# Optimization experiments

Measured on AMD Instinct MI355X. Metric: run time of the kernel, lower is better.

Reference implementation:

```python
import jax, jax.numpy as jnp
import numpy as np

EPS = 1e-08
CLAMP = 10.0


def setup_inputs() -> dict:
    key = jax.random.key(0)
    ks = jax.random.split(key, 16)
    B, T, F, H = 128, 512, 256, 512
    s_in = 1.0 / np.sqrt(F)
    s_h = 1.0 / np.sqrt(H)
    inp = {
        "x": jax.random.normal(ks[0], (B, T, F), dtype=jnp.float32),
        "Wf": jax.random.normal(ks[1], (F, H), dtype=jnp.float32) * s_in,
        "bf": jax.random.normal(ks[2], (H,), dtype=jnp.float32) * s_in,
        "Wi": jax.random.normal(ks[3], (F, H), dtype=jnp.float32) * s_in,
        "bi": jax.random.normal(ks[4], (H,), dtype=jnp.float32) * s_in,
        "Wo": jax.random.normal(ks[5], (F, H), dtype=jnp.float32) * s_in,
        "bo": jax.random.normal(ks[6], (H,), dtype=jnp.float32) * s_in,
        "Wz": jax.random.normal(ks[7], (F, H), dtype=jnp.float32) * s_in,
        "bz": jax.random.normal(ks[8], (H,), dtype=jnp.float32) * s_in,
        "Rf": jax.random.normal(ks[9], (H, H), dtype=jnp.float32) * s_h,
        "Ri": jax.random.normal(ks[10], (H, H), dtype=jnp.float32) * s_h,
        "Ro": jax.random.normal(ks[11], (H, H), dtype=jnp.float32) * s_h,
        "Rz": jax.random.normal(ks[12], (H, H), dtype=jnp.float32) * s_h,
        "fc_w": jax.random.normal(ks[13], (H, 1), dtype=jnp.float32) * s_h,
        "fc_b": jax.random.normal(ks[14], (1,), dtype=jnp.float32) * s_h,
    }
    return inp


def _slstm_forward(x, Wf, bf, Wi, bi, Wo, bo, Wz, bz, Rf, Ri, Ro, Rz, fc_w, fc_b):
    B, T, F = x.shape
    H = Wf.shape[1]
    # Precompute all input projections in one batched GEMM pass: [B,T,H] each
    xf = jnp.einsum("btf,fh->bth", x, Wf) + bf
    xi = jnp.einsum("btf,fh->bth", x, Wi) + bi
    xo = jnp.einsum("btf,fh->bth", x, Wo) + bo
    xz = jnp.einsum("btf,fh->bth", x, Wz) + bz
    # Stack time-major for scan: [T, B, H]
    xs = jnp.stack([xf, xi, xo, xz], axis=0).transpose(2, 0, 1, 3)  # [T,4,B,H]

    def step(carry, xt):
        h, c, n = carry
        xf_t, xi_t, xo_t, xz_t = xt[0], xt[1], xt[2], xt[3]
        f_tilde = xf_t + h @ Rf
        i_tilde = xi_t + h @ Ri
        o = jax.nn.sigmoid(xo_t + h @ Ro)
        z = jnp.tanh(xz_t + h @ Rz)
        f_hat = jnp.exp(jnp.minimum(f_tilde, CLAMP))
        i_hat = jnp.exp(jnp.minimum(i_tilde, CLAMP))
        denom = f_hat + i_hat + EPS
        f = f_hat / denom
        i = i_hat / denom
        c = f * c + i * z
        n = f * n + i
        h = o * (c / (n + EPS))
        return (h, c, n), None

    zeros = jnp.zeros((B, H), dtype=x.dtype)
    (h, _, _), _ = jax.lax.scan(step, (zeros, zeros, zeros), xs)
    # dropout is identity at inference
    pos = jnp.tanh(h @ fc_w + fc_b)  # [B,1]
    return pos.squeeze(-1)  # [B]


def reference(x, Wf, bf, Wi, bi, Wo, bo, Wz, bz, Rf, Ri, Ro, Rz, fc_w, fc_b):
    return _slstm_forward(x, Wf, bf, Wi, bi, Wo, bo, Wz, bz, Rf, Ri, Ro, Rz, fc_w, fc_b)
```

## Files before the change

kernel.cpp:

```cpp
#include <hip/hip_runtime.h>

constexpr int Bdim = 128;
constexpr int Tdim = 512;
constexpr int Fdim = 256;
constexpr int Hdim = 512;
constexpr int Kdim = Fdim + Hdim;
constexpr int NB   = 8;
constexpr int CC   = 128;
constexpr int NC   = 8;
constexpr int NK   = 24;
constexpr float EPSc = 1e-8f;
constexpr float CLAMPc = 10.0f;

constexpr size_t FLAGS_BYTES = 32768;

typedef _Float16 half2v __attribute__((ext_vector_type(2)));
typedef _Float16 half4v __attribute__((ext_vector_type(4)));

__device__ __forceinline__ float wave_sum4(float v) {
    v += __shfl_xor(v, 16);
    v += __shfl_xor(v, 32);
    return v;
}

__global__ __launch_bounds__(512, 2) void slstm_persist(
    const float* __restrict__ x,
    const float* __restrict__ Wf, const float* __restrict__ bfv,
    const float* __restrict__ Wi, const float* __restrict__ biv,
    const float* __restrict__ Wo, const float* __restrict__ bov,
    const float* __restrict__ Wz, const float* __restrict__ bzv,
    const float* __restrict__ Rf, const float* __restrict__ Ri,
    const float* __restrict__ Ro, const float* __restrict__ Rz,
    const float* __restrict__ fcw, const float* __restrict__ fcb,
    int* flags, unsigned long long* hbuf,
    float* __restrict__ out)
{
    const int tid  = threadIdx.x;
    const int xcd  = blockIdx.x & 7;
    const int slot = blockIdx.x >> 3;
    const int bb   = xcd * 2 + (slot & 1);
    const int jb   = slot >> 1;

    const int kg   = tid >> 4;
    const int colg = tid & 15;
    const int k0   = kg * NK;

    half2v wpk[NC][NK / 2];
    #pragma unroll
    for (int ci = 0; ci < NC; ++ci) {
        const int cc   = colg * NC + ci;
        const int g    = cc >> 5;
        const int hcol = jb * 32 + (cc & 31);
        const float* Wg = (g == 0) ? Wf : (g == 1) ? Wi : (g == 2) ? Wo : Wz;
        const float* Rg = (g == 0) ? Rf : (g == 1) ? Ri : (g == 2) ? Ro : Rz;
        #pragma unroll
        for (int j = 0; j < NK / 2; ++j) {
            const int k = k0 + 2 * j;
            float w0, w1;
            if (k < Fdim) {
                w0 = Wg[(size_t)k * Hdim + hcol];
                w1 = Wg[(size_t)(k + 1) * Hdim + hcol];
            } else {
                w0 = Rg[(size_t)(k - Fdim) * Hdim + hcol];
                w1 = Rg[(size_t)(k + 1 - Fdim) * Hdim + hcol];
            }
            wpk[ci][j] = half2v{(_Float16)w0, (_Float16)w1};
        }
    }

    const int ub  = tid >> 5;
    const int uhc = tid & 31;
    float bias_f = 0.f, bias_i = 0.f, bias_o = 0.f, bias_z = 0.f;
    if (tid < 256) {
        bias_f = bfv[jb * 32 + uhc];
        bias_i = biv[jb * 32 + uhc];
        bias_o = bov[jb * 32 + uhc];
        bias_z = bzv[jb * 32 + uhc];
    }
    float c_st = 0.f, n_st = 0.f;

    __shared__ _Float16 in_s[NB][Kdim];
    __shared__ float    part_s[8][NB][CC];

    {
        const int b  = tid >> 6;
        const int f4 = tid & 63;
        float4 v = *reinterpret_cast<const float4*>(
            x + ((size_t)(bb * NB + b) * Tdim + 0) * Fdim + f4 * 4);
        *reinterpret_cast<half4v*>(&in_s[b][f4 * 4]) =
            half4v{(_Float16)v.x, (_Float16)v.y, (_Float16)v.z, (_Float16)v.w};
        const int row = tid >> 6;
        const int u0  = (tid & 63) * 2;
        *reinterpret_cast<unsigned long long*>(&in_s[row][Fdim + u0 * 4])     = 0ull;
        *reinterpret_cast<unsigned long long*>(&in_s[row][Fdim + u0 * 4 + 4]) = 0ull;
    }
    __syncthreads();

    for (int t = 0; t < Tdim; ++t) {
        float acc[NC][NB];
        #pragma unroll
        for (int ci = 0; ci < NC; ++ci)
            #pragma unroll
            for (int b = 0; b < NB; ++b) acc[ci][b] = 0.f;

        #pragma unroll
        for (int b = 0; b < NB; ++b) {
            const half2v* p = reinterpret_cast<const half2v*>(&in_s[b][k0]);
            half2v hp[12];
            #pragma unroll
            for (int j = 0; j < 12; ++j) hp[j] = p[j];
            #pragma unroll
            for (int ci = 0; ci < NC; ++ci) {
                #pragma unroll
                for (int j = 0; j < NK / 2; ++j) {
                    acc[ci][b] = __builtin_amdgcn_fdot2(
                        wpk[ci][j], hp[j], acc[ci][b], false);
                }
            }
        }

        #pragma unroll
        for (int ci = 0; ci < NC; ++ci)
            #pragma unroll
            for (int b = 0; b < NB; ++b)
                acc[ci][b] = wave_sum4(acc[ci][b]);

        {
            const int wv  = tid >> 6;
            const int kgl = (tid >> 4) & 3;
            #pragma unroll
            for (int bs = 0; bs < 2; ++bs) {
                const int b = kgl * 2 + bs;
                #pragma unroll
                for (int cp = 0; cp < NC / 2; ++cp) {
                    float2 w2 = make_float2(acc[2 * cp][b], acc[2 * cp + 1][b]);
                    *reinterpret_cast<float2*>(&part_s[wv][b][colg * NC + 2 * cp]) = w2;
                }
            }
        }
        __syncthreads();

        if (tid < 256) {
            float pre[4];
            #pragma unroll
            for (int g = 0; g < 4; ++g) {
                float s = 0.f;
                #pragma unroll
                for (int w = 0; w < 8; ++w) s += part_s[w][ub][g * 32 + uhc];
                pre[g] = s;
            }
            pre[0] += bias_f; pre[1] += bias_i; pre[2] += bias_o; pre[3] += bias_z;

            float o  = 1.0f / (1.0f + __expf(-pre[2]));
            float z  = tanhf(pre[3]);
            float fh = __expf(fminf(pre[0], CLAMPc));
            float ih = __expf(fminf(pre[1], CLAMPc));
            float denom = fh + ih + EPSc;
            float f  = fh / denom;
            float ii = ih / denom;
            c_st = f * c_st + ii * z;
            n_st = f * n_st + ii;
            float hval = o * (c_st / (n_st + EPSc));

            float h1 = __shfl_xor(hval, 1);
            half2v hp2 = half2v{(_Float16)hval, (_Float16)h1};
            unsigned pck = __builtin_bit_cast(unsigned, hp2);
            unsigned qck = (unsigned)__shfl_xor((int)pck, 2);
            if ((uhc & 3) == 0) {
                unsigned long long v64 =
                    (unsigned long long)pck | ((unsigned long long)qck << 32);
                __hip_atomic_store(
                    &hbuf[(((size_t)(t & 1) * 16 + bb) * 8 + ub) * 128 + ((jb * 32 + uhc) >> 2)],
                    v64, __ATOMIC_RELAXED, __HIP_MEMORY_SCOPE_AGENT);
            }
        }

        if (t + 1 < Tdim) {
            const int b  = tid >> 6;
            const int f4 = tid & 63;
            float4 v = *reinterpret_cast<const float4*>(
                x + ((size_t)(bb * NB + b) * Tdim + (t + 1)) * Fdim + f4 * 4);
            *reinterpret_cast<half4v*>(&in_s[b][f4 * 4]) =
                half4v{(_Float16)v.x, (_Float16)v.y, (_Float16)v.z, (_Float16)v.w};
        }

        __syncthreads();

        if (tid == 0)
            __hip_atomic_store(&flags[(bb * 16 + jb) * 32], t + 1,
                               __ATOMIC_RELAXED, __HIP_MEMORY_SCOPE_AGENT);
        if (tid < 16) {
            while (__hip_atomic_load(&flags[(bb * 16 + tid) * 32],
                                     __ATOMIC_RELAXED, __HIP_MEMORY_SCOPE_AGENT) < t + 1) {}
        }
        __syncthreads();

        {
            const int row = tid >> 6;
            const int u0  = (tid & 63) * 2;
            unsigned long long* src =
                &hbuf[(((size_t)(t & 1) * 16 + bb) * 8 + row) * 128];
            unsigned long long a = __hip_atomic_load(&src[u0],
                                __ATOMIC_RELAXED, __HIP_MEMORY_SCOPE_AGENT);
            unsigned long long b = __hip_atomic_load(&src[u0 + 1],
                                __ATOMIC_RELAXED, __HIP_MEMORY_SCOPE_AGENT);
            *reinterpret_cast<unsigned long long*>(&in_s[row][Fdim + u0 * 4])     = a;
            *reinterpret_cast<unsigned long long*>(&in_s[row][Fdim + u0 * 4 + 4]) = b;
        }
        __syncthreads();
    }

    if (jb == 0) {
        const int w = tid >> 6;
        const int l = tid & 63;
        float p = 0.f;
        #pragma unroll
        for (int s = 0; s < 8; ++s)
            p += (float)in_s[w][Fdim + l + s * 64] * fcw[l + s * 64];
        p += __shfl_xor(p, 32);
        p += __shfl_xor(p, 16);
        p += __shfl_xor(p, 8);
        p += __shfl_xor(p, 4);
        p += __shfl_xor(p, 2);
        p += __shfl_xor(p, 1);
        if (l == 0) out[bb * NB + w] = tanhf(p + fcb[0]);
    }
}

extern "C" void kernel_launch(void* const* d_in, const int* in_sizes, int n_in,
                              void* d_out, int out_size, void* d_ws, size_t ws_size,
                              hipStream_t stream) {
    const float* x   = (const float*)d_in[0];
    const float* Wf  = (const float*)d_in[1];
    const float* bf_ = (const float*)d_in[2];
    const float* Wi  = (const float*)d_in[3];
    const float* bi_ = (const float*)d_in[4];
    const float* Wo  = (const float*)d_in[5];
    const float* bo_ = (const float*)d_in[6];
    const float* Wz  = (const float*)d_in[7];
    const float* bz_ = (const float*)d_in[8];
    const float* Rf  = (const float*)d_in[9];
    const float* Ri  = (const float*)d_in[10];
    const float* Ro  = (const float*)d_in[11];
    const float* Rz  = (const float*)d_in[12];
    const float* fcw = (const float*)d_in[13];
    const float* fcb = (const float*)d_in[14];

    int* flags = (int*)d_ws;
    unsigned long long* hbuf =
        (unsigned long long*)((char*)d_ws + FLAGS_BYTES);
    float* o = (float*)d_out;

    hipMemsetAsync(d_ws, 0, FLAGS_BYTES, stream);

    void* args[] = { &x, &Wf, &bf_, &Wi, &bi_, &Wo, &bo_, &Wz, &bz_,
                     &Rf, &Ri, &Ro, &Rz, &fcw, &fcb, &flags, &hbuf, &o };

    hipLaunchCooperativeKernel(reinterpret_cast<void*>(slstm_persist),
                               dim3(256), dim3(512), args, 0, stream);
}
```

Baseline: 4.970 ms.

## Replace flag barrier with sentinel-polled triple-buffered hidden-state exchange

Drops the per-block flag counters and the two-phase spin barrier. Consumers now poll the hidden-state buffer itself with cache-bypassing 128-bit loads until no sentinel value remains, and the buffer is triple-buffered so slots can be reset to the sentinel one step ahead. The next timestep's x load is issued early and written to shared memory after the first barrier, which removes one __syncthreads per step. The aim is to cut the barrier and flag round-trip latency on the sequential critical path. The risk is that correctness depends on an fp16 h pair never matching the all-ones sentinel and on the inline-asm cache-bypass semantics.

```diff
diff --git a/kernel.cpp b/kernel.cpp
--- a/kernel.cpp
+++ b/kernel.cpp
@@ -12,15 +12,25 @@
 constexpr float EPSc = 1e-8f;
 constexpr float CLAMPc = 10.0f;
 
-constexpr size_t FLAGS_BYTES = 32768;
+constexpr unsigned long long SENT = 0xFFFFFFFFFFFFFFFFull;
+constexpr size_t HBUF_U64 = (size_t)3 * 16 * 8 * 128;
 
 typedef _Float16 half2v __attribute__((ext_vector_type(2)));
 typedef _Float16 half4v __attribute__((ext_vector_type(4)));
+typedef unsigned long long u64x2 __attribute__((ext_vector_type(2)));
 
 __device__ __forceinline__ float wave_sum4(float v) {
     v += __shfl_xor(v, 16);
     v += __shfl_xor(v, 32);
     return v;
+}
+
+__device__ __forceinline__ u64x2 load_b128_bypass(const unsigned long long* p) {
+    u64x2 r;
+    asm volatile("global_load_dwordx4 %0, %1, off sc0 sc1 nt\n\t"
+                 "s_waitcnt vmcnt(0)"
+                 : "=v"(r) : "v"(p) : "memory");
+    return r;
 }
 
 __global__ __launch_bounds__(512, 2) void slstm_persist(
@@ -32,7 +42,7 @@
     const float* __restrict__ Rf, const float* __restrict__ Ri,
     const float* __restrict__ Ro, const float* __restrict__ Rz,
     const float* __restrict__ fcw, const float* __restrict__ fcb,
-    int* flags, unsigned long long* hbuf,
+    unsigned long long* hbuf,
     float* __restrict__ out)
 {
     const int tid  = threadIdx.x;
@@ -79,6 +89,9 @@
     }
     float c_st = 0.f, n_st = 0.f;
 
+    const int grow = tid >> 6;
+    const int gu0  = (tid & 63) * 2;
+
     __shared__ _Float16 in_s[NB][Kdim];
     __shared__ float    part_s[8][NB][CC];
 
@@ -89,14 +102,21 @@
             x + ((size_t)(bb * NB + b) * Tdim + 0) * Fdim + f4 * 4);
         *reinterpret_cast<half4v*>(&in_s[b][f4 * 4]) =
             half4v{(_Float16)v.x, (_Float16)v.y, (_Float16)v.z, (_Float16)v.w};
-        const int row = tid >> 6;
-        const int u0  = (tid & 63) * 2;
-        *reinterpret_cast<unsigned long long*>(&in_s[row][Fdim + u0 * 4])     = 0ull;
-        *reinterpret_cast<unsigned long long*>(&in_s[row][Fdim + u0 * 4 + 4]) = 0ull;
+        *reinterpret_cast<unsigned long long*>(&in_s[grow][Fdim + gu0 * 4])     = 0ull;
+        *reinterpret_cast<unsigned long long*>(&in_s[grow][Fdim + gu0 * 4 + 4]) = 0ull;
     }
     __syncthreads();
 
     for (int t = 0; t < Tdim; ++t) {
+        const int tn = (t + 1 < Tdim) ? (t + 1) : (Tdim - 1);
+        float4 xnext = *reinterpret_cast<const float4*>(
+            x + ((size_t)(bb * NB + (tid >> 6)) * Tdim + tn) * Fdim + (tid & 63) * 4);
+
+        if (tid < 64) {
+            hbuf[((((size_t)(t + 1) % 3) * 16 + bb) * 8 + (tid >> 3)) * 128
+                 + jb * 8 + (tid & 7)] = SENT;
+        }
+
         float acc[NC][NB];
         #pragma unroll
         for (int ci = 0; ci < NC; ++ci)
@@ -139,6 +159,12 @@
             }
         }
         __syncthreads();
+
+        {
+            *reinterpret_cast<half4v*>(&in_s[tid >> 6][(tid & 63) * 4]) =
+                half4v{(_Float16)xnext.x, (_Float16)xnext.y,
+                       (_Float16)xnext.z, (_Float16)xnext.w};
+        }
 
         if (tid < 256) {
             float pre[4];
@@ -170,42 +196,21 @@
                 unsigned long long v64 =
                     (unsigned long long)pck | ((unsigned long long)qck << 32);
                 __hip_atomic_store(
-                    &hbuf[(((size_t)(t & 1) * 16 + bb) * 8 + ub) * 128 + ((jb * 32 + uhc) >> 2)],
+                    &hbuf[(((size_t)(t % 3) * 16 + bb) * 8 + ub) * 128
+                          + ((jb * 32 + uhc) >> 2)],
                     v64, __ATOMIC_RELAXED, __HIP_MEMORY_SCOPE_AGENT);
             }
         }
 
-        if (t + 1 < Tdim) {
-            const int b  = tid >> 6;
-            const int f4 = tid & 63;
-            float4 v = *reinterpret_cast<const float4*>(
-                x + ((size_t)(bb * NB + b) * Tdim + (t + 1)) * Fdim + f4 * 4);
-            *reinterpret_cast<half4v*>(&in_s[b][f4 * 4]) =
-                half4v{(_Float16)v.x, (_Float16)v.y, (_Float16)v.z, (_Float16)v.w};
-        }
-
-        __syncthreads();
-
-        if (tid == 0)
-            __hip_atomic_store(&flags[(bb * 16 + jb) * 32], t + 1,
-                               __ATOMIC_RELAXED, __HIP_MEMORY_SCOPE_AGENT);
-        if (tid < 16) {
-            while (__hip_atomic_load(&flags[(bb * 16 + tid) * 32],
-                                     __ATOMIC_RELAXED, __HIP_MEMORY_SCOPE_AGENT) < t + 1) {}
-        }
-        __syncthreads();
-
         {
-            const int row = tid >> 6;
-            const int u0  = (tid & 63) * 2;
-            unsigned long long* src =
-                &hbuf[(((size_t)(t & 1) * 16 + bb) * 8 + row) * 128];
-            unsigned long long a = __hip_atomic_load(&src[u0],
-                                __ATOMIC_RELAXED, __HIP_MEMORY_SCOPE_AGENT);
-            unsigned long long b = __hip_atomic_load(&src[u0 + 1],
-                                __ATOMIC_RELAXED, __HIP_MEMORY_SCOPE_AGENT);
-            *reinterpret_cast<unsigned long long*>(&in_s[row][Fdim + u0 * 4])     = a;
-            *reinterpret_cast<unsigned long long*>(&in_s[row][Fdim + u0 * 4 + 4]) = b;
+            const unsigned long long* src =
+                &hbuf[(((size_t)(t % 3) * 16 + bb) * 8 + grow) * 128 + gu0];
+            u64x2 v;
+            do {
+                v = load_b128_bypass(src);
+            } while (v.x == SENT || v.y == SENT);
+            *reinterpret_cast<unsigned long long*>(&in_s[grow][Fdim + gu0 * 4])     = v.x;
+            *reinterpret_cast<unsigned long long*>(&in_s[grow][Fdim + gu0 * 4 + 4]) = v.y;
         }
         __syncthreads();
     }
@@ -246,15 +251,13 @@
     const float* fcw = (const float*)d_in[13];
     const float* fcb = (const float*)d_in[14];
 
-    int* flags = (int*)d_ws;
-    unsigned long long* hbuf =
-        (unsigned long long*)((char*)d_ws + FLAGS_BYTES);
+    unsigned long long* hbuf = (unsigned long long*)d_ws;
     float* o = (float*)d_out;
 
-    hipMemsetAsync(d_ws, 0, FLAGS_BYTES, stream);
+    hipMemsetAsync(d_ws, 0xFF, HBUF_U64 * sizeof(unsigned long long), stream);
 
     void* args[] = { &x, &Wf, &bf_, &Wi, &bi_, &Wo, &bo_, &Wz, &bz_,
-                     &Rf, &Ri, &Ro, &Rz, &fcw, &fcb, &flags, &hbuf, &o };
+                     &Rf, &Ri, &Ro, &Rz, &fcw, &fcb, &hbuf, &o };
 
     hipLaunchCooperativeKernel(reinterpret_cast<void*>(slstm_persist),
                                dim3(256), dim3(512), args, 0, stream);
```

After: 6.822 ms. 1.37x slower.
